# Optimization experiments

Hardware: AMD Instinct MI355X
Metric: run time of the kernel (lower is better)

The kernel has to match this reference:

```python
import jax, jax.numpy as jnp
import numpy as np

D = 768      # embed_dim
P = 16       # patch size
NP = 14      # patches per side
L = 197      # seq len (196 patches + CLS)
H = 12       # heads
HD = D // H  # head dim
DEPTH = 12
B = 32
ALPHA = 0.5
EPS = 1e-5


def layer_norm(x, g, b):
    m = x.mean(-1, keepdims=True)
    v = ((x - m) ** 2).mean(-1, keepdims=True)
    return g * (x - m) / jnp.sqrt(v + EPS) + b


def patch_embed(x, w, b, g, beta):
    # x: [B, C, 224, 224]; w: [D, C, P, P] (Conv2d stride=P == patchify + matmul)
    Bx, C = x.shape[0], x.shape[1]
    p = x.reshape(Bx, C, NP, P, NP, P).transpose(0, 2, 4, 1, 3, 5).reshape(Bx, NP * NP, C * P * P)
    t = p @ w.reshape(D, -1).T + b
    return layer_norm(t, g, beta)


def setup_inputs() -> dict:
    key = jax.random.key(0)
    ks = jax.random.split(key, 24)
    rn = lambda k, shape, s=0.02: (jax.random.normal(k, shape, jnp.float32) * s)
    inp = {
        'img': jax.random.normal(ks[0], (B, 3, 224, 224), jnp.float32),
        'mask': jax.random.uniform(ks[1], (B, 224, 224), jnp.float32),
        'pe_img_w': rn(ks[2], (D, 3, P, P)), 'pe_img_b': jnp.zeros((D,), jnp.float32),
        'pe_img_g': jnp.ones((D,), jnp.float32), 'pe_img_bb': jnp.zeros((D,), jnp.float32),
        'pe_msk_w': rn(ks[3], (D, 1, P, P)), 'pe_msk_b': jnp.zeros((D,), jnp.float32),
        'pe_msk_g': jnp.ones((D,), jnp.float32), 'pe_msk_bb': jnp.zeros((D,), jnp.float32),
        'cls': rn(ks[4], (1, 1, D)),
        'pos': rn(ks[5], (1, L, D)),
        'ln1_g': jnp.ones((DEPTH, D), jnp.float32), 'ln1_b': jnp.zeros((DEPTH, D), jnp.float32),
        'w_qkv': rn(ks[6], (DEPTH, 3 * D, D)), 'b_qkv': jnp.zeros((DEPTH, 3 * D), jnp.float32),
        'w_out': rn(ks[7], (DEPTH, D, D)), 'b_out': jnp.zeros((DEPTH, D), jnp.float32),
        'ln2_g': jnp.ones((DEPTH, D), jnp.float32), 'ln2_b': jnp.zeros((DEPTH, D), jnp.float32),
        'w_fc1': rn(ks[8], (DEPTH, 4 * D, D)), 'b_fc1': jnp.zeros((DEPTH, 4 * D), jnp.float32),
        'w_fc2': rn(ks[9], (DEPTH, D, 4 * D)), 'b_fc2': jnp.zeros((DEPTH, D), jnp.float32),
        'enc_g': jnp.ones((D,), jnp.float32), 'enc_b': jnp.zeros((D,), jnp.float32),
        'fin_g': jnp.ones((D,), jnp.float32), 'fin_b': jnp.zeros((D,), jnp.float32),
        'head_w': rn(ks[10], (4, D)), 'head_b': jnp.zeros((4,), jnp.float32),
    }
    return inp


def reference(img, mask, pe_img_w, pe_img_b, pe_img_g, pe_img_bb,
              pe_msk_w, pe_msk_b, pe_msk_g, pe_msk_bb, cls, pos,
              ln1_g, ln1_b, w_qkv, b_qkv, w_out, b_out, ln2_g, ln2_b,
              w_fc1, b_fc1, w_fc2, b_fc2, enc_g, enc_b, fin_g, fin_b,
              head_w, head_b):
    Bx = img.shape[0]
    tok_i = patch_embed(img, pe_img_w, pe_img_b, pe_img_g, pe_img_bb)
    tok_m = patch_embed(mask[:, None], pe_msk_w, pe_msk_b, pe_msk_g, pe_msk_bb)
    tokens = tok_i + ALPHA * tok_m                       # [B, 196, D]
    x = jnp.concatenate([jnp.broadcast_to(cls, (Bx, 1, D)), tokens], axis=1) + pos  # [B, L, D]
    # low-rank outer-product attention bias, zero on CLS row/col
    bias_p = jnp.einsum('bid,bjd->bij', tok_m, tok_m) / jnp.sqrt(jnp.float32(D))
    bias = jnp.pad(bias_p, ((0, 0), (1, 0), (1, 0)))     # [B, L, L]

    def block(x, p):
        l1g, l1b, wqkv, bqkv, wo, bo, l2g, l2b, w1, b1, w2, b2 = p
        h = layer_norm(x, l1g, l1b)
        qkv = h @ wqkv.T + bqkv                          # [B, L, 3D]
        q, k, v = jnp.split(qkv, 3, axis=-1)
        hds = lambda t: t.reshape(Bx, L, H, HD).transpose(0, 2, 1, 3)
        q, k, v = hds(q), hds(k), hds(v)                 # [B, H, L, HD]
        s = jnp.einsum('bhid,bhjd->bhij', q, k) / jnp.sqrt(jnp.float32(HD)) + bias[:, None]
        a = jax.nn.softmax(s, axis=-1)
        o = jnp.einsum('bhij,bhjd->bhid', a, v).transpose(0, 2, 1, 3).reshape(Bx, L, D)
        x = x + o @ wo.T + bo
        h2 = layer_norm(x, l2g, l2b)
        x = x + jax.nn.gelu(h2 @ w1.T + b1, approximate=False) @ w2.T + b2
        return x, None

    x, _ = jax.lax.scan(block, x, (ln1_g, ln1_b, w_qkv, b_qkv, w_out, b_out,
                                   ln2_g, ln2_b, w_fc1, b_fc1, w_fc2, b_fc2))
    x = layer_norm(x, enc_g, enc_b)   # ViTEncoder.norm
    x = layer_norm(x, fin_g, fin_b)   # MaskedViT.norm
    return x[:, 0] @ head_w.T + head_b  # [B, num_classes]
```

## Files before the change

### kernel.cpp

```cpp
#include <hip/hip_runtime.h>
#include <hip/hip_bf16.h>
#include <math.h>

typedef unsigned int   u32;
typedef unsigned short u16;
typedef __bf16 bf16x8 __attribute__((ext_vector_type(8)));
typedef float  f32x4  __attribute__((ext_vector_type(4)));
typedef u16    u16x8  __attribute__((ext_vector_type(8)));
typedef u16    u16x4  __attribute__((ext_vector_type(4)));

constexpr int BB = 32, DD = 768, LL = 197, HH = 12, NTOK = 196;
constexpr int MROWS = BB * LL;
constexpr int MTOK  = BB * NTOK;

__device__ __forceinline__ u16 f2bf(float f) {
    union { float f; u32 u; } v; v.f = f;
    u32 r = v.u + 0x7fff + ((v.u >> 16) & 1);
    return (u16)(r >> 16);
}
__device__ __forceinline__ float bf2f(u16 u) {
    union { u32 u; float f; } v; v.u = ((u32)u) << 16;
    return v.f;
}

#define AS1 __attribute__((address_space(1)))
#define AS3 __attribute__((address_space(3)))
__device__ __forceinline__ void gload_lds16(const void* g, void* l) {
    __builtin_amdgcn_global_load_lds((const AS1 u32*)g, (AS3 u32*)l, 16, 0, 0);
}

__global__ void cast_kernel(const float* __restrict__ in, u16* __restrict__ out, int n)
{
    int i4 = (blockIdx.x * 256 + threadIdx.x) * 4;
    if (i4 >= n) return;
    float4 v = *reinterpret_cast<const float4*>(in + i4);
    out[i4]   = f2bf(v.x); out[i4+1] = f2bf(v.y);
    out[i4+2] = f2bf(v.z); out[i4+3] = f2bf(v.w);
}

__global__ void cast4_kernel(const float* s0, int n0, const float* s1, int n1,
                             const float* s2, int n2, const float* s3, int n3,
                             u16* d0, u16* d1, u16* d2, u16* d3)
{
    int i4 = (blockIdx.x * 256 + threadIdx.x) * 4;
    const float* s; u16* d; int off;
    if      (i4 < n0)            { s = s0; d = d0; off = i4; }
    else if (i4 < n0+n1)         { s = s1; d = d1; off = i4 - n0; }
    else if (i4 < n0+n1+n2)      { s = s2; d = d2; off = i4 - n0 - n1; }
    else if (i4 < n0+n1+n2+n3)   { s = s3; d = d3; off = i4 - n0 - n1 - n2; }
    else return;
    float4 v = *reinterpret_cast<const float4*>(s + off);
    d[off]   = f2bf(v.x); d[off+1] = f2bf(v.y);
    d[off+2] = f2bf(v.z); d[off+3] = f2bf(v.w);
}

__global__ void patchify_kernel(const float* __restrict__ src, int C,
                                u16* __restrict__ out, int total)
{
    int idx = blockIdx.x * 256 + threadIdx.x;
    if (idx >= total) return;
    int K = C * 256;
    int row = idx / K, k = idx % K;
    int b = row / NTOK, n = row % NTOK;
    int c = k >> 8, rem = k & 255, pi = rem >> 4, pj = rem & 15;
    int i14 = n / 14, j14 = n % 14;
    float v = src[(((size_t)b * C + c) * 224 + i14 * 16 + pi) * 224 + j14 * 16 + pj];
    out[idx] = f2bf(v);
}

template<int MODE>
__global__ __launch_bounds__(256) void gemm_bf16(
    const u16* __restrict__ A, const u16* __restrict__ W,
    const float* __restrict__ bias, const float* __restrict__ res,
    void* __restrict__ Cout, int M, int N, int K, long long strideA)
{
    __shared__ u16 As[128 * 32];
    __shared__ u16 Bs[128 * 32];
    const int tid  = threadIdx.x;
    const int wave = tid >> 6, lane = tid & 63;
    const int lo = lane & 15, hi = lane >> 4;
    const int wr = wave >> 1, wc = wave & 1;

    const int m0 = blockIdx.y * 128, n0 = blockIdx.x * 128;
    if (MODE == 3) { A += blockIdx.z * strideA; W += blockIdx.z * strideA; }

    const int Klen = (MODE == 5) ? (K >> 1) : K;
    const int kb   = (MODE == 5) ? blockIdx.z * Klen : 0;

    const int limA = M - 1;
    const int limB = (MODE == 3 ? M : N) - 1;
    const int srow = lane >> 2;
    const int scol = ((lane & 3) ^ ((lane >> 3) & 3)) << 3;
    int ra0 = m0 + wave * 16 + srow;      if (ra0 > limA) ra0 = limA;
    int ra1 = m0 + 64 + wave * 16 + srow; if (ra1 > limA) ra1 = limA;
    int rb0 = n0 + wave * 16 + srow;      if (rb0 > limB) rb0 = limB;
    int rb1 = n0 + 64 + wave * 16 + srow; if (rb1 > limB) rb1 = limB;
    const u16* Arow0 = A + (size_t)ra0 * K + kb + scol;
    const u16* Arow1 = A + (size_t)ra1 * K + kb + scol;
    const u16* Brow0 = W + (size_t)rb0 * K + kb + scol;
    const u16* Brow1 = W + (size_t)rb1 * K + kb + scol;

    u16* ldsA0 = &As[wave * 512];
    u16* ldsA1 = &As[2048 + wave * 512];
    u16* ldsB0 = &Bs[wave * 512];
    u16* ldsB1 = &Bs[2048 + wave * 512];

    const int fro = lo * 32 + ((hi ^ ((lo >> 1) & 3)) << 3);

    f32x4 acc[4][4] = {};

    for (int k0 = 0; k0 < Klen; k0 += 32) {
        gload_lds16(Arow0 + k0, ldsA0);
        gload_lds16(Arow1 + k0, ldsA1);
        gload_lds16(Brow0 + k0, ldsB0);
        gload_lds16(Brow1 + k0, ldsB1);
        __syncthreads();
        bf16x8 af[4], bfr[4];
        #pragma unroll
        for (int i = 0; i < 4; ++i)
            af[i] = *reinterpret_cast<const bf16x8*>(&As[(wr * 4 + i) * 512 + fro]);
        #pragma unroll
        for (int j = 0; j < 4; ++j)
            bfr[j] = *reinterpret_cast<const bf16x8*>(&Bs[(wc * 4 + j) * 512 + fro]);
        #pragma unroll
        for (int i = 0; i < 4; ++i)
            #pragma unroll
            for (int j = 0; j < 4; ++j)
                acc[i][j] = __builtin_amdgcn_mfma_f32_16x16x32_bf16(af[i], bfr[j], acc[i][j], 0, 0, 0);
        __syncthreads();
    }

    const size_t zoff = (MODE == 5) ? (size_t)blockIdx.z * M * N : 0;
    const int cr = hi * 4;
    const int cc = lo;
    #pragma unroll
    for (int i = 0; i < 4; ++i) {
        #pragma unroll
        for (int r = 0; r < 4; ++r) {
            int m = m0 + wr * 64 + i * 16 + cr + r;
            if (MODE != 3 && m >= M) continue;
            #pragma unroll
            for (int j = 0; j < 4; ++j) {
                int n = n0 + wc * 64 + j * 16 + cc;
                float v = acc[i][j][r];
                if (MODE == 0) {
                    ((float*)Cout)[(size_t)m * N + n] = v + bias[n];
                } else if (MODE == 1) {
                    float t = v + bias[n];
                    t = 0.5f * t * (1.f + erff(t * 0.70710678118654752f));
                    ((u16*)Cout)[(size_t)m * N + n] = f2bf(t);
                } else if (MODE == 2) {
                    ((float*)Cout)[(size_t)m * N + n] = v + bias[n] + res[(size_t)m * N + n];
                } else if (MODE == 4) {
                    ((u16*)Cout)[(size_t)m * N + n] = f2bf(v + bias[n]);
                } else if (MODE == 5) {
                    ((float*)Cout)[zoff + (size_t)m * N + n] = v;
                } else {
                    if (m < M && n < M) {
                        float* C3 = (float*)Cout + (size_t)blockIdx.z * LL * LL;
                        C3[(size_t)(m + 1) * LL + (n + 1)] = v * 0.03608439182435161f;
                    }
                }
            }
        }
    }
}

__global__ void splitk_reduce_kernel(float* __restrict__ x, const float* __restrict__ p,
                                     const float* __restrict__ bias, int MN, int N)
{
    int i4 = (blockIdx.x * 256 + threadIdx.x) * 4;
    if (i4 >= MN) return;
    float4 a  = *reinterpret_cast<const float4*>(x + i4);
    float4 p0 = *reinterpret_cast<const float4*>(p + i4);
    float4 p1 = *reinterpret_cast<const float4*>(p + (size_t)MN + i4);
    float4 b  = *reinterpret_cast<const float4*>(bias + (i4 % N));
    a.x += p0.x + p1.x + b.x;
    a.y += p0.y + p1.y + b.y;
    a.z += p0.z + p1.z + b.z;
    a.w += p0.w + p1.w + b.w;
    *reinterpret_cast<float4*>(x + i4) = a;
}

__global__ void bias_edge_kernel(float* __restrict__ bias)
{
    int b = blockIdx.x, t = threadIdx.x;
    if (t < LL) {
        bias[((size_t)b * LL + 0) * LL + t] = 0.f;
        bias[((size_t)b * LL + t) * LL + 0] = 0.f;
    }
}

__global__ void combine_kernel(
    const float* __restrict__ toki, const float* __restrict__ tokm,
    const float* __restrict__ cls, const float* __restrict__ pos,
    float* __restrict__ x)
{
    size_t idx = (size_t)blockIdx.x * 256 + threadIdx.x;
    if (idx >= (size_t)MROWS * DD) return;
    int d = (int)(idx % DD);
    size_t bl = idx / DD;
    int l = (int)(bl % LL);
    int b = (int)(bl / LL);
    float v;
    if (l == 0) v = cls[d];
    else {
        size_t tix = ((size_t)b * NTOK + (l - 1)) * DD + d;
        v = toki[tix] + 0.5f * tokm[tix];
    }
    x[idx] = v + pos[(size_t)l * DD + d];
}

template<int OUT>
__global__ __launch_bounds__(256) void ln_kernel(
    const float* __restrict__ in, const float* __restrict__ g,
    const float* __restrict__ beta, float* __restrict__ outf,
    u16* __restrict__ outb, int nrows)
{
    int row = blockIdx.x * 4 + (threadIdx.x >> 6);
    if (row >= nrows) return;
    int lane = threadIdx.x & 63;
    const float* xr = in + (size_t)row * DD;
    float4 v[3];
    #pragma unroll
    for (int p = 0; p < 3; ++p)
        v[p] = *reinterpret_cast<const float4*>(xr + p * 256 + lane * 4);
    float s = 0.f;
    #pragma unroll
    for (int p = 0; p < 3; ++p) s += v[p].x + v[p].y + v[p].z + v[p].w;
    #pragma unroll
    for (int off = 32; off; off >>= 1) s += __shfl_xor(s, off);
    float mean = s * (1.f / 768.f);
    float q = 0.f;
    #pragma unroll
    for (int p = 0; p < 3; ++p) {
        float a = v[p].x - mean, b = v[p].y - mean, c = v[p].z - mean, d = v[p].w - mean;
        q += a * a + b * b + c * c + d * d;
    }
    #pragma unroll
    for (int off = 32; off; off >>= 1) q += __shfl_xor(q, off);
    float rstd = rsqrtf(q * (1.f / 768.f) + 1e-5f);
    #pragma unroll
    for (int p = 0; p < 3; ++p) {
        int d0 = p * 256 + lane * 4;
        float4 gg = *reinterpret_cast<const float4*>(g + d0);
        float4 bb = *reinterpret_cast<const float4*>(beta + d0);
        float o0 = gg.x * (v[p].x - mean) * rstd + bb.x;
        float o1 = gg.y * (v[p].y - mean) * rstd + bb.y;
        float o2 = gg.z * (v[p].z - mean) * rstd + bb.z;
        float o3 = gg.w * (v[p].w - mean) * rstd + bb.w;
        if (OUT == 0 || OUT == 2) {
            float4 of = make_float4(o0, o1, o2, o3);
            *reinterpret_cast<float4*>(outf + (size_t)row * DD + d0) = of;
        }
        if (OUT == 1 || OUT == 2) {
            u16x4 ob = { f2bf(o0), f2bf(o1), f2bf(o2), f2bf(o3) };
            *reinterpret_cast<u16x4*>(outb + (size_t)row * DD + d0) = ob;
        }
    }
}

constexpr int KSTRE = 72;
constexpr int VSTRE = 232;
constexpr int PSTRE = 232;

__global__ __launch_bounds__(512) void attn_mfma_kernel(
    const u16* __restrict__ qkv, const float* __restrict__ bias,
    u16* __restrict__ o)
{
    const int h = blockIdx.x, b = blockIdx.y;
    const int tid = threadIdx.x, wave = tid >> 6, lane = tid & 63;
    const int lo = lane & 15, hi = lane >> 4;

    __shared__ u16 Ks[208 * KSTRE];
    __shared__ u16 Vt[64 * VSTRE];
    __shared__ u16 Ps[8][16 * PSTRE];

    const u16* qb = qkv + (size_t)b * LL * 2304;

    for (int idx = tid; idx < 208 * 8; idx += 512) {
        int key = idx >> 3, c8 = idx & 7;
        u16x8 v = {};
        if (key < LL) v = *reinterpret_cast<const u16x8*>(qb + (size_t)key * 2304 + 768 + h * 64 + c8 * 8);
        *reinterpret_cast<u16x8*>(&Ks[key * KSTRE + c8 * 8]) = v;
    }
    for (int idx = tid; idx < 224 * 8; idx += 512) {
        int key = idx >> 3, c8 = idx & 7;
        u16x8 v = {};
        if (key < LL) v = *reinterpret_cast<const u16x8*>(qb + (size_t)key * 2304 + 1536 + h * 64 + c8 * 8);
        #pragma unroll
        for (int e = 0; e < 8; ++e) Vt[(c8 * 8 + e) * VSTRE + key] = v[e];
    }
    __syncthreads();

    u16* P = Ps[wave];
    const float* biasbb = bias + (size_t)b * LL * LL;

    for (int rt = wave; rt < 13; rt += 8) {
        int q = rt * 16 + lo; if (q > LL - 1) q = LL - 1;
        const u16* qrow = qb + (size_t)q * 2304 + h * 64;
        bf16x8 qa0 = *reinterpret_cast<const bf16x8*>(qrow + hi * 8);
        bf16x8 qa1 = *reinterpret_cast<const bf16x8*>(qrow + 32 + hi * 8);

        f32x4 st[13];
        #pragma unroll
        for (int t = 0; t < 13; ++t) {
            int keyc = t * 16 + lo;
            bf16x8 kb0 = *reinterpret_cast<const bf16x8*>(&Ks[keyc * KSTRE + hi * 8]);
            bf16x8 kb1 = *reinterpret_cast<const bf16x8*>(&Ks[keyc * KSTRE + 32 + hi * 8]);
            f32x4 a = {};
            a = __builtin_amdgcn_mfma_f32_16x16x32_bf16(qa0, kb0, a, 0, 0, 0);
            a = __builtin_amdgcn_mfma_f32_16x16x32_bf16(qa1, kb1, a, 0, 0, 0);
            st[t] = a;
        }

        #pragma unroll
        for (int r = 0; r < 4; ++r) {
            int qq = rt * 16 + hi * 4 + r;
            int qc = qq > LL - 1 ? LL - 1 : qq;
            const float* brow = biasbb + (size_t)qc * LL;
            float s[13];
            float m = -1e30f;
            #pragma unroll
            for (int t = 0; t < 13; ++t) {
                int col = t * 16 + lo;
                float v;
                if (col < LL) v = st[t][r] * 0.125f + brow[col];
                else          v = -1e30f;
                s[t] = v;
                m = fmaxf(m, v);
            }
            m = fmaxf(m, __shfl_xor(m, 1));
            m = fmaxf(m, __shfl_xor(m, 2));
            m = fmaxf(m, __shfl_xor(m, 4));
            m = fmaxf(m, __shfl_xor(m, 8));
            float sum = 0.f;
            #pragma unroll
            for (int t = 0; t < 13; ++t) { float e = __expf(s[t] - m); s[t] = e; sum += e; }
            sum += __shfl_xor(sum, 1);
            sum += __shfl_xor(sum, 2);
            sum += __shfl_xor(sum, 4);
            sum += __shfl_xor(sum, 8);
            float inv = 1.f / sum;
            int prow = (hi * 4 + r) * PSTRE;
            #pragma unroll
            for (int t = 0; t < 13; ++t) P[prow + t * 16 + lo] = f2bf(s[t] * inv);
            P[prow + 208 + lo] = 0;
        }

        f32x4 oacc[4] = {};
        #pragma unroll
        for (int kt = 0; kt < 7; ++kt) {
            bf16x8 pa = *reinterpret_cast<const bf16x8*>(&P[lo * PSTRE + kt * 32 + hi * 8]);
            #pragma unroll
            for (int dt = 0; dt < 4; ++dt) {
                bf16x8 vb = *reinterpret_cast<const bf16x8*>(&Vt[(dt * 16 + lo) * VSTRE + kt * 32 + hi * 8]);
                oacc[dt] = __builtin_amdgcn_mfma_f32_16x16x32_bf16(pa, vb, oacc[dt], 0, 0, 0);
            }
        }

        #pragma unroll
        for (int dt = 0; dt < 4; ++dt) {
            #pragma unroll
            for (int r = 0; r < 4; ++r) {
                int qq = rt * 16 + hi * 4 + r;
                if (qq < LL)
                    o[((size_t)(b * LL + qq)) * DD + h * 64 + dt * 16 + lo] = f2bf(oacc[dt][r]);
            }
        }
    }
}

__global__ __launch_bounds__(256) void final_kernel(
    const float* __restrict__ x,
    const float* __restrict__ eg, const float* __restrict__ eb,
    const float* __restrict__ fg, const float* __restrict__ fb,
    const float* __restrict__ hw, const float* __restrict__ hb,
    float* __restrict__ out)
{
    int b = blockIdx.x;
    int tid = threadIdx.x;
    __shared__ float xs[768];
    __shared__ float red[256];
    const float* xr = x + (size_t)b * LL * DD;
    #pragma unroll
    for (int r = 0; r < 3; ++r) xs[tid + r * 256] = xr[tid + r * 256];
    __syncthreads();
    for (int pass = 0; pass < 2; ++pass) {
        const float* g  = pass ? fg : eg;
        const float* bb = pass ? fb : eb;
        red[tid] = xs[tid] + xs[tid + 256] + xs[tid + 512];
        __syncthreads();
        for (int off = 128; off; off >>= 1) {
            if (tid < off) red[tid] += red[tid + off];
            __syncthreads();
        }
        float mean = red[0] * (1.f / 768.f);
        __syncthreads();
        float q = 0.f;
        #pragma unroll
        for (int r = 0; r < 3; ++r) { float dv = xs[tid + r * 256] - mean; q += dv * dv; }
        red[tid] = q;
        __syncthreads();
        for (int off = 128; off; off >>= 1) {
            if (tid < off) red[tid] += red[tid + off];
            __syncthreads();
        }
        float rstd = rsqrtf(red[0] * (1.f / 768.f) + 1e-5f);
        __syncthreads();
        #pragma unroll
        for (int r = 0; r < 3; ++r) {
            int d = tid + r * 256;
            xs[d] = g[d] * (xs[d] - mean) * rstd + bb[d];
        }
        __syncthreads();
    }
    int c = tid >> 6, lane = tid & 63;
    float part = 0.f;
    for (int d = lane; d < 768; d += 64) part += xs[d] * hw[c * 768 + d];
    #pragma unroll
    for (int off = 32; off; off >>= 1) part += __shfl_down(part, off);
    if (lane == 0) out[b * 4 + c] = part + hb[c];
}

extern "C" void kernel_launch(void* const* d_in, const int* in_sizes, int n_in,
                              void* d_out, int out_size, void* d_ws, size_t ws_size,
                              hipStream_t stream)
{
    const float* img    = (const float*)d_in[0];
    const float* mask   = (const float*)d_in[1];
    const float* pe_iw  = (const float*)d_in[2];
    const float* pe_ib  = (const float*)d_in[3];
    const float* pe_ig  = (const float*)d_in[4];
    const float* pe_ibb = (const float*)d_in[5];
    const float* pe_mw  = (const float*)d_in[6];
    const float* pe_mb  = (const float*)d_in[7];
    const float* pe_mg  = (const float*)d_in[8];
    const float* pe_mbb = (const float*)d_in[9];
    const float* cls    = (const float*)d_in[10];
    const float* pos    = (const float*)d_in[11];
    const float* ln1_g  = (const float*)d_in[12];
    const float* ln1_b  = (const float*)d_in[13];
    const float* w_qkv  = (const float*)d_in[14];
    const float* b_qkv  = (const float*)d_in[15];
    const float* w_out  = (const float*)d_in[16];
    const float* b_out  = (const float*)d_in[17];
    const float* ln2_g  = (const float*)d_in[18];
    const float* ln2_b  = (const float*)d_in[19];
    const float* w_fc1  = (const float*)d_in[20];
    const float* b_fc1  = (const float*)d_in[21];
    const float* w_fc2  = (const float*)d_in[22];
    const float* b_fc2  = (const float*)d_in[23];
    const float* enc_g  = (const float*)d_in[24];
    const float* enc_b  = (const float*)d_in[25];
    const float* fin_g  = (const float*)d_in[26];
    const float* fin_b  = (const float*)d_in[27];
    const float* head_w = (const float*)d_in[28];
    const float* head_b = (const float*)d_in[29];

    char* wsb = (char*)d_ws;
    size_t off = 0;
    auto alloc = [&](size_t bytes) { void* p = wsb + off; off += (bytes + 255) & ~(size_t)255; return p; };

    float* x     = (float*)alloc((size_t)MROWS * DD * 4);
    u16*   qkvb  = (u16*)  alloc((size_t)MROWS * 3 * DD * 2);
    u16*   hbuf  = (u16*)  alloc((size_t)MROWS * DD * 2);
    u16*   fc1b  = (u16*)  alloc((size_t)MROWS * 4 * DD * 2);
    float* biasb = (float*)alloc((size_t)BB * LL * LL * 4);
    u16*   wqb   = (u16*)  alloc((size_t)3 * DD * DD * 2);
    u16*   wob   = (u16*)  alloc((size_t)DD * DD * 2);
    u16*   w1b   = (u16*)  alloc((size_t)4 * DD * DD * 2);
    u16*   w2b   = (u16*)  alloc((size_t)4 * DD * DD * 2);
    float* toki  = (float*)alloc((size_t)MTOK * DD * 4);
    float* tokm  = (float*)alloc((size_t)MTOK * DD * 4);
    u16*   pa    = fc1b;
    float* ttmp  = (float*)qkvb;
    u16*   tokmb = hbuf;
    float* partf = (float*)qkvb;

    cast_kernel<<<(DD * DD / 4 + 255) / 256, 256, 0, stream>>>(pe_iw, wob, DD * DD);
    patchify_kernel<<<(MTOK * DD + 255) / 256, 256, 0, stream>>>(img, 3, pa, MTOK * DD);
    gemm_bf16<0><<<dim3(DD / 128, MTOK / 128), 256, 0, stream>>>(
        pa, wob, pe_ib, nullptr, ttmp, MTOK, DD, DD, 0);
    ln_kernel<0><<<MTOK / 4, 256, 0, stream>>>(ttmp, pe_ig, pe_ibb, toki, nullptr, MTOK);

    cast_kernel<<<(DD * 256 / 4 + 255) / 256, 256, 0, stream>>>(pe_mw, wob, DD * 256);
    patchify_kernel<<<(MTOK * 256 + 255) / 256, 256, 0, stream>>>(mask, 1, pa, MTOK * 256);
    gemm_bf16<0><<<dim3(DD / 128, MTOK / 128), 256, 0, stream>>>(
        pa, wob, pe_mb, nullptr, ttmp, MTOK, DD, 256, 0);
    ln_kernel<2><<<MTOK / 4, 256, 0, stream>>>(ttmp, pe_mg, pe_mbb, tokm, tokmb, MTOK);

    gemm_bf16<3><<<dim3(2, 2, BB), 256, 0, stream>>>(
        tokmb, tokmb, nullptr, nullptr, biasb, NTOK, NTOK, DD, (long long)NTOK * DD);
    bias_edge_kernel<<<BB, 256, 0, stream>>>(biasb);

    combine_kernel<<<(MROWS * DD + 255) / 256, 256, 0, stream>>>(toki, tokm, cls, pos, x);

    const int mblk = (MROWS + 127) / 128;
    const int MN = MROWS * DD;
    const int wqn = 3 * DD * DD, won = DD * DD, w1n = 4 * DD * DD, w2n = 4 * DD * DD;
    const int castTot = (wqn + won + w1n + w2n) / 4;
    for (int l = 0; l < 12; ++l) {
        cast4_kernel<<<(castTot + 255) / 256, 256, 0, stream>>>(
            w_qkv + (size_t)l * wqn, wqn, w_out + (size_t)l * won, won,
            w_fc1 + (size_t)l * w1n, w1n, w_fc2 + (size_t)l * w2n, w2n,
            wqb, wob, w1b, w2b);
        ln_kernel<1><<<MROWS / 4, 256, 0, stream>>>(x, ln1_g + l * DD, ln1_b + l * DD, nullptr, hbuf, MROWS);
        gemm_bf16<4><<<dim3(3 * DD / 128, mblk), 256, 0, stream>>>(
            hbuf, wqb, b_qkv + l * 3 * DD, nullptr, qkvb, MROWS, 3 * DD, DD, 0);
        attn_mfma_kernel<<<dim3(HH, BB), 512, 0, stream>>>(qkvb, biasb, hbuf);
        gemm_bf16<2><<<dim3(DD / 128, mblk), 256, 0, stream>>>(
            hbuf, wob, b_out + l * DD, x, x, MROWS, DD, DD, 0);
        ln_kernel<1><<<MROWS / 4, 256, 0, stream>>>(x, ln2_g + l * DD, ln2_b + l * DD, nullptr, hbuf, MROWS);
        gemm_bf16<1><<<dim3(4 * DD / 128, mblk), 256, 0, stream>>>(
            hbuf, w1b, b_fc1 + l * 4 * DD, nullptr, fc1b, MROWS, 4 * DD, DD, 0);
        gemm_bf16<5><<<dim3(DD / 128, mblk, 2), 256, 0, stream>>>(
            fc1b, w2b, nullptr, nullptr, partf, MROWS, DD, 4 * DD, 0);
        splitk_reduce_kernel<<<(MN / 4 + 255) / 256, 256, 0, stream>>>(
            x, partf, b_fc2 + l * DD, MN, DD);
    }
    final_kernel<<<BB, 256, 0, stream>>>(x, enc_g, enc_b, fin_g, fin_b, head_w, head_b, (float*)d_out);
}
```

Measured before the change: 3.441 ms.

## Double-buffer GEMM LDS tiles and fuse split-K reduce with next LayerNorm

The GEMM main loop now ping-pongs between two LDS buffers, so the global-to-LDS load of the next K tile is issued before computing on the current tile, and one barrier per tile is removed. The split-K reduction of FC2 is fused with the following layer's LN1 into one kernel, which drops a separate LayerNorm pass over x per layer. The partial buffer moves to a dedicated scratch area shared with the patch-embed tokens. LDS use doubles, which may lower occupancy.

```diff
diff --git a/kernel.cpp b/kernel.cpp
--- a/kernel.cpp
+++ b/kernel.cpp
@@ -74,8 +74,8 @@
     const float* __restrict__ bias, const float* __restrict__ res,
     void* __restrict__ Cout, int M, int N, int K, long long strideA)
 {
-    __shared__ u16 As[128 * 32];
-    __shared__ u16 Bs[128 * 32];
+    __shared__ u16 As[2][4096];
+    __shared__ u16 Bs[2][4096];
     const int tid  = threadIdx.x;
     const int wave = tid >> 6, lane = tid & 63;
     const int lo = lane & 15, hi = lane >> 4;
@@ -100,35 +100,55 @@
     const u16* Brow0 = W + (size_t)rb0 * K + kb + scol;
     const u16* Brow1 = W + (size_t)rb1 * K + kb + scol;
 
-    u16* ldsA0 = &As[wave * 512];
-    u16* ldsA1 = &As[2048 + wave * 512];
-    u16* ldsB0 = &Bs[wave * 512];
-    u16* ldsB1 = &Bs[2048 + wave * 512];
-
     const int fro = lo * 32 + ((hi ^ ((lo >> 1) & 3)) << 3);
 
     f32x4 acc[4][4] = {};
 
-    for (int k0 = 0; k0 < Klen; k0 += 32) {
-        gload_lds16(Arow0 + k0, ldsA0);
-        gload_lds16(Arow1 + k0, ldsA1);
-        gload_lds16(Brow0 + k0, ldsB0);
-        gload_lds16(Brow1 + k0, ldsB1);
+    #define STAGE(bf_, k0_)                                        \
+        do {                                                       \
+            gload_lds16(Arow0 + (k0_), &As[bf_][wave * 512]);      \
+            gload_lds16(Arow1 + (k0_), &As[bf_][2048 + wave * 512]);\
+            gload_lds16(Brow0 + (k0_), &Bs[bf_][wave * 512]);      \
+            gload_lds16(Brow1 + (k0_), &Bs[bf_][2048 + wave * 512]);\
+        } while (0)
+
+    #define COMPUTE(bf_)                                                         \
+        do {                                                                     \
+            bf16x8 af[4], bfr[4];                                                \
+            _Pragma("unroll")                                                    \
+            for (int i = 0; i < 4; ++i)                                          \
+                af[i] = *reinterpret_cast<const bf16x8*>(                        \
+                    &As[bf_][(wr * 4 + i) * 512 + fro]);                         \
+            _Pragma("unroll")                                                    \
+            for (int j = 0; j < 4; ++j)                                          \
+                bfr[j] = *reinterpret_cast<const bf16x8*>(                       \
+                    &Bs[bf_][(wc * 4 + j) * 512 + fro]);                         \
+            _Pragma("unroll")                                                    \
+            for (int i = 0; i < 4; ++i)                                          \
+                _Pragma("unroll")                                                \
+                for (int j = 0; j < 4; ++j)                                      \
+                    acc[i][j] = __builtin_amdgcn_mfma_f32_16x16x32_bf16(         \
+                        af[i], bfr[j], acc[i][j], 0, 0, 0);                      \
+        } while (0)
+
+    const int nt = Klen >> 5;
+    STAGE(0, 0);
+    __syncthreads();
+    int t = 0;
+    for (; t + 2 < nt; t += 2) {
+        STAGE(1, (t + 1) * 32);
+        COMPUTE(0);
         __syncthreads();
-        bf16x8 af[4], bfr[4];
-        #pragma unroll
-        for (int i = 0; i < 4; ++i)
-            af[i] = *reinterpret_cast<const bf16x8*>(&As[(wr * 4 + i) * 512 + fro]);
-        #pragma unroll
-        for (int j = 0; j < 4; ++j)
-            bfr[j] = *reinterpret_cast<const bf16x8*>(&Bs[(wc * 4 + j) * 512 + fro]);
-        #pragma unroll
-        for (int i = 0; i < 4; ++i)
-            #pragma unroll
-            for (int j = 0; j < 4; ++j)
-                acc[i][j] = __builtin_amdgcn_mfma_f32_16x16x32_bf16(af[i], bfr[j], acc[i][j], 0, 0, 0);
+        STAGE(0, (t + 2) * 32);
+        COMPUTE(1);
         __syncthreads();
     }
+    STAGE(1, (t + 1) * 32);
+    COMPUTE(0);
+    __syncthreads();
+    COMPUTE(1);
+    #undef STAGE
+    #undef COMPUTE
 
     const size_t zoff = (MODE == 5) ? (size_t)blockIdx.z * M * N : 0;
     const int cr = hi * 4;
@@ -146,9 +166,9 @@
                 if (MODE == 0) {
                     ((float*)Cout)[(size_t)m * N + n] = v + bias[n];
                 } else if (MODE == 1) {
-                    float t = v + bias[n];
-                    t = 0.5f * t * (1.f + erff(t * 0.70710678118654752f));
-                    ((u16*)Cout)[(size_t)m * N + n] = f2bf(t);
+                    float t2 = v + bias[n];
+                    t2 = 0.5f * t2 * (1.f + erff(t2 * 0.70710678118654752f));
+                    ((u16*)Cout)[(size_t)m * N + n] = f2bf(t2);
                 } else if (MODE == 2) {
                     ((float*)Cout)[(size_t)m * N + n] = v + bias[n] + res[(size_t)m * N + n];
                 } else if (MODE == 4) {
@@ -180,6 +200,60 @@
     a.z += p0.z + p1.z + b.z;
     a.w += p0.w + p1.w + b.w;
     *reinterpret_cast<float4*>(x + i4) = a;
+}
+
+__global__ __launch_bounds__(256) void reduce_ln_kernel(
+    float* __restrict__ x, const float* __restrict__ p,
+    const float* __restrict__ bias,
+    const float* __restrict__ g, const float* __restrict__ beta,
+    u16* __restrict__ outb, int nrows)
+{
+    int row = blockIdx.x * 4 + (threadIdx.x >> 6);
+    if (row >= nrows) return;
+    int lane = threadIdx.x & 63;
+    size_t MN = (size_t)nrows * DD;
+    float4 v[3];
+    #pragma unroll
+    for (int pp = 0; pp < 3; ++pp) {
+        int d0 = pp * 256 + lane * 4;
+        size_t ix = (size_t)row * DD + d0;
+        float4 xv = *reinterpret_cast<const float4*>(x + ix);
+        float4 p0 = *reinterpret_cast<const float4*>(p + ix);
+        float4 p1 = *reinterpret_cast<const float4*>(p + MN + ix);
+        float4 bv = *reinterpret_cast<const float4*>(bias + d0);
+        xv.x += p0.x + p1.x + bv.x;
+        xv.y += p0.y + p1.y + bv.y;
+        xv.z += p0.z + p1.z + bv.z;
+        xv.w += p0.w + p1.w + bv.w;
+        *reinterpret_cast<float4*>(x + ix) = xv;
+        v[pp] = xv;
+    }
+    float s = 0.f;
+    #pragma unroll
+    for (int pp = 0; pp < 3; ++pp) s += v[pp].x + v[pp].y + v[pp].z + v[pp].w;
+    #pragma unroll
+    for (int off = 32; off; off >>= 1) s += __shfl_xor(s, off);
+    float mean = s * (1.f / 768.f);
+    float q = 0.f;
+    #pragma unroll
+    for (int pp = 0; pp < 3; ++pp) {
+        float a = v[pp].x - mean, b = v[pp].y - mean, c = v[pp].z - mean, d = v[pp].w - mean;
+        q += a * a + b * b + c * c + d * d;
+    }
+    #pragma unroll
+    for (int off = 32; off; off >>= 1) q += __shfl_xor(q, off);
+    float rstd = rsqrtf(q * (1.f / 768.f) + 1e-5f);
+    #pragma unroll
+    for (int pp = 0; pp < 3; ++pp) {
+        int d0 = pp * 256 + lane * 4;
+        float4 gg = *reinterpret_cast<const float4*>(g + d0);
+        float4 bb = *reinterpret_cast<const float4*>(beta + d0);
+        u16x4 ob = { f2bf(gg.x * (v[pp].x - mean) * rstd + bb.x),
+                     f2bf(gg.y * (v[pp].y - mean) * rstd + bb.y),
+                     f2bf(gg.z * (v[pp].z - mean) * rstd + bb.z),
+                     f2bf(gg.w * (v[pp].w - mean) * rstd + bb.w) };
+        *reinterpret_cast<u16x4*>(outb + (size_t)row * DD + d0) = ob;
+    }
 }
 
 __global__ void bias_edge_kernel(float* __restrict__ bias)
@@ -471,12 +545,13 @@
     u16*   wob   = (u16*)  alloc((size_t)DD * DD * 2);
     u16*   w1b   = (u16*)  alloc((size_t)4 * DD * DD * 2);
     u16*   w2b   = (u16*)  alloc((size_t)4 * DD * DD * 2);
-    float* toki  = (float*)alloc((size_t)MTOK * DD * 4);
-    float* tokm  = (float*)alloc((size_t)MTOK * DD * 4);
+    float* scratch2 = (float*)alloc((size_t)2 * MROWS * DD * 4);
+    float* toki  = scratch2;
+    float* tokm  = scratch2 + (size_t)MTOK * DD;
+    float* partf = scratch2;
     u16*   pa    = fc1b;
     float* ttmp  = (float*)qkvb;
     u16*   tokmb = hbuf;
-    float* partf = (float*)qkvb;
 
     cast_kernel<<<(DD * DD / 4 + 255) / 256, 256, 0, stream>>>(pe_iw, wob, DD * DD);
     patchify_kernel<<<(MTOK * DD + 255) / 256, 256, 0, stream>>>(img, 3, pa, MTOK * DD);
@@ -495,6 +570,7 @@
     bias_edge_kernel<<<BB, 256, 0, stream>>>(biasb);
 
     combine_kernel<<<(MROWS * DD + 255) / 256, 256, 0, stream>>>(toki, tokm, cls, pos, x);
+    ln_kernel<1><<<MROWS / 4, 256, 0, stream>>>(x, ln1_g, ln1_b, nullptr, hbuf, MROWS);
 
     const int mblk = (MROWS + 127) / 128;
     const int MN = MROWS * DD;
@@ -505,7 +581,6 @@
             w_qkv + (size_t)l * wqn, wqn, w_out + (size_t)l * won, won,
             w_fc1 + (size_t)l * w1n, w1n, w_fc2 + (size_t)l * w2n, w2n,
             wqb, wob, w1b, w2b);
-        ln_kernel<1><<<MROWS / 4, 256, 0, stream>>>(x, ln1_g + l * DD, ln1_b + l * DD, nullptr, hbuf, MROWS);
         gemm_bf16<4><<<dim3(3 * DD / 128, mblk), 256, 0, stream>>>(
             hbuf, wqb, b_qkv + l * 3 * DD, nullptr, qkvb, MROWS, 3 * DD, DD, 0);
         attn_mfma_kernel<<<dim3(HH, BB), 512, 0, stream>>>(qkvb, biasb, hbuf);
@@ -516,8 +591,14 @@
             hbuf, w1b, b_fc1 + l * 4 * DD, nullptr, fc1b, MROWS, 4 * DD, DD, 0);
         gemm_bf16<5><<<dim3(DD / 128, mblk, 2), 256, 0, stream>>>(
             fc1b, w2b, nullptr, nullptr, partf, MROWS, DD, 4 * DD, 0);
-        splitk_reduce_kernel<<<(MN / 4 + 255) / 256, 256, 0, stream>>>(
-            x, partf, b_fc2 + l * DD, MN, DD);
+        if (l < 11) {
+            reduce_ln_kernel<<<MROWS / 4, 256, 0, stream>>>(
+                x, partf, b_fc2 + l * DD, ln1_g + (l + 1) * DD, ln1_b + (l + 1) * DD,
+                hbuf, MROWS);
+        } else {
+            splitk_reduce_kernel<<<(MN / 4 + 255) / 256, 256, 0, stream>>>(
+                x, partf, b_fc2 + l * DD, MN, DD);
+        }
     }
     final_kernel<<<BB, 256, 0, stream>>>(x, enc_g, enc_b, fin_g, fin_b, head_w, head_b, (float*)d_out);
 }
```

New measurement: 3.247 ms. -5.6%, faster.
